# Performance work log

Hardware: AMD Instinct MI355X
Metric: run time of the kernel (lower is better)

Reference implementation:

```python
import jax, jax.numpy as jnp
import numpy as np

N_NODES = 1024
H = 256        # hidden_dim
HEADS = 4
EPS = 1e-5     # torch LayerNorm default


def _ln(x, g, b):
    m = x.mean(-1, keepdims=True)
    v = ((x - m) ** 2).mean(-1, keepdims=True)
    return (x - m) / jnp.sqrt(v + EPS) * g + b


def setup_inputs() -> dict:
    key = jax.random.key(0)
    ks = jax.random.split(key, 24)
    B, L = 16, 64
    P = N_NODES * (N_NODES - 1) // 2
    D0 = L + 7  # latent_dim + 7 stats
    s = 0.02
    f32 = jnp.float32
    d = {}
    d['x'] = jax.random.normal(ks[0], (B, L), f32)
    d['stats'] = jax.random.normal(ks[1], (B, 7), f32)
    d['u'] = jax.random.uniform(ks[2], (B, P, 2), f32)  # uniform noise -> gumbel
    d['ln0_g'] = jnp.ones((D0,), f32); d['ln0_b'] = jnp.zeros((D0,), f32)
    # residual block 1 (in D0 -> H, has projection)
    d['rb1_ln_g'] = jnp.ones((D0,), f32); d['rb1_ln_b'] = jnp.zeros((D0,), f32)
    d['rb1_w1'] = jax.random.normal(ks[3], (H, D0), f32) * s; d['rb1_b1'] = jnp.zeros((H,), f32)
    d['rb1_w2'] = jax.random.normal(ks[4], (H, H), f32) * s;  d['rb1_b2'] = jnp.zeros((H,), f32)
    d['rb1_wp'] = jax.random.normal(ks[5], (H, D0), f32) * s; d['rb1_bp'] = jnp.zeros((H,), f32)
    # residual block 2 (H -> H, no projection)
    d['rb2_ln_g'] = jnp.ones((H,), f32); d['rb2_ln_b'] = jnp.zeros((H,), f32)
    d['rb2_w1'] = jax.random.normal(ks[6], (H, H), f32) * s; d['rb2_b1'] = jnp.zeros((H,), f32)
    d['rb2_w2'] = jax.random.normal(ks[7], (H, H), f32) * s; d['rb2_b2'] = jnp.zeros((H,), f32)
    # GraphAttention: LN + MHA(in_proj, out_proj) + output Linear
    d['att_ln_g'] = jnp.ones((H,), f32); d['att_ln_b'] = jnp.zeros((H,), f32)
    d['att_win'] = jax.random.normal(ks[8], (3 * H, H), f32) * s; d['att_bin'] = jnp.zeros((3 * H,), f32)
    d['att_wout'] = jax.random.normal(ks[9], (H, H), f32) * s;    d['att_bout'] = jnp.zeros((H,), f32)
    d['out_w'] = jax.random.normal(ks[10], (H, H), f32) * s;      d['out_b'] = jnp.zeros((H,), f32)
    # final edge-logit layer over concat([h_i, h_j]) -> 2
    d['fin_w'] = jax.random.normal(ks[11], (2, 2 * H), f32) * s;  d['fin_b'] = jnp.zeros((2,), f32)
    d['temp'] = jnp.ones((1,), f32)
    return d


def reference(x, stats, u, ln0_g, ln0_b,
              rb1_ln_g, rb1_ln_b, rb1_w1, rb1_b1, rb1_w2, rb1_b2, rb1_wp, rb1_bp,
              rb2_ln_g, rb2_ln_b, rb2_w1, rb2_b1, rb2_w2, rb2_b2,
              att_ln_g, att_ln_b, att_win, att_bin, att_wout, att_bout,
              out_w, out_b, fin_w, fin_b, temp):
    B = x.shape[0]
    z = jnp.concatenate([x, stats], axis=-1)          # [B, D0]
    z = _ln(z, ln0_g, ln0_b)
    h = jnp.broadcast_to(z[:, None, :], (B, N_NODES, z.shape[-1]))  # [B, N, D0]
    # residual block 1 (dropout in eval mode = identity)
    t = _ln(h, rb1_ln_g, rb1_ln_b)
    t = jax.nn.gelu(t @ rb1_w1.T + rb1_b1, approximate=False)
    t = t @ rb1_w2.T + rb1_b2
    h = t + (h @ rb1_wp.T + rb1_bp)                   # [B, N, H]
    # residual block 2
    t = _ln(h, rb2_ln_g, rb2_ln_b)
    t = jax.nn.gelu(t @ rb2_w1.T + rb2_b1, approximate=False)
    t = t @ rb2_w2.T + rb2_b2
    h = t + h
    # GraphAttention: LN -> self MHA -> output linear
    a = _ln(h, att_ln_g, att_ln_b)
    qkv = a @ att_win.T + att_bin                      # [B, N, 3H]
    q, k, v = jnp.split(qkv, 3, axis=-1)
    dh = H // HEADS
    def heads(t):
        return t.reshape(B, N_NODES, HEADS, dh).transpose(0, 2, 1, 3)
    q, k, v = heads(q), heads(k), heads(v)
    scores = jnp.einsum('bhqd,bhkd->bhqk', q, k) * np.float32(1.0 / np.sqrt(dh))
    att = jax.nn.softmax(scores, axis=-1)
    o = jnp.einsum('bhqk,bhkd->bhqd', att, v).transpose(0, 2, 1, 3).reshape(B, N_NODES, H)
    o = o @ att_wout.T + att_bout
    h = o @ out_w.T + out_b                            # [B, N, H]
    # pairwise edge logits: Linear(cat(h_i, h_j)) == h_i @ W_a^T + h_j @ W_b^T + b
    la = h @ fin_w[:, :H].T                            # [B, N, 2]
    lb = h @ fin_w[:, H:].T                            # [B, N, 2]
    iu, ju = jnp.triu_indices(N_NODES, k=1)
    logits = la[:, iu] + lb[:, ju] + fin_b             # [B, P, 2]
    # gumbel-softmax (hard, straight-through), tau = |temperature|
    tau = jnp.abs(temp)[0]
    g = -jnp.log(-jnp.log(u + 1e-10) + 1e-10)
    y_soft = jax.nn.softmax((logits + g) / tau, axis=-1)
    y_hard = jax.nn.one_hot(jnp.argmax(y_soft, axis=-1), 2, dtype=y_soft.dtype)
    y = y_hard + y_soft - jax.lax.stop_gradient(y_soft)
    e = y[..., 0]                                      # [B, P]
    adj = jnp.zeros((B, N_NODES, N_NODES), e.dtype).at[:, iu, ju].set(e)
    return adj + adj.transpose(0, 2, 1)
```

## Files before the change

### kernel.cpp

```cpp
#include <hip/hip_runtime.h>
#include <math.h>


#define NN    1024
#define HD    256
#define DIN0  71
#define NPAIR 523776
#define TILE  64
#define NT    16

__device__ __forceinline__ double bred(double v, double* red4) {
  #pragma unroll
  for (int m = 32; m > 0; m >>= 1) v += __shfl_xor(v, m, 64);
  const int wid = threadIdx.x >> 6;
  __syncthreads();
  if ((threadIdx.x & 63) == 0) red4[wid] = v;
  __syncthreads();
  return (red4[0] + red4[1]) + (red4[2] + red4[3]);
}

__device__ __forceinline__ double quad_sum(double v) {
  v += __shfl_xor(v, 1, 64);
  v += __shfl_xor(v, 2, 64);
  return v;
}

__device__ __forceinline__ double dotq256(const double* s,
                                          const float* __restrict__ W,
                                          int row, int p) {
  const float4* w4 = reinterpret_cast<const float4*>(W + (size_t)row * 256);
  double a0 = 0.0, a1 = 0.0, a2 = 0.0, a3 = 0.0;
  #pragma unroll
  for (int k = 0; k < 16; ++k) {
    const int f = p + 4 * k;
    float4 w = w4[f];
    const double* sp = s + 4 * f;
    a0 += sp[0] * (double)w.x;
    a1 += sp[1] * (double)w.y;
    a2 += sp[2] * (double)w.z;
    a3 += sp[3] * (double)w.w;
  }
  return (a0 + a1) + (a2 + a3);
}

__device__ __forceinline__ double dotq71(const double* s,
                                         const float* __restrict__ W,
                                         int row, int p) {
  const float* wr = W + (size_t)row * DIN0;
  double a = 0.0;
  #pragma unroll
  for (int i = p; i < DIN0; i += 4) a += s[i] * (double)wr[i];
  return a;
}

__device__ __forceinline__ double gelu_exact(double x) {
  return 0.5 * x * (1.0 + erf(x * 0.70710678118654752440));
}

__device__ __forceinline__ void ln0_into(const float* __restrict__ x,
                                         const float* __restrict__ stats,
                                         const float* __restrict__ g,
                                         const float* __restrict__ bb,
                                         int b, double* h0, double* red4) {
  const int tid = threadIdx.x;
  double z = 0.0;
  if (tid < DIN0)
    z = (tid < 64) ? (double)x[b * 64 + tid] : (double)stats[b * 7 + tid - 64];
  const double m = bred((tid < DIN0) ? z : 0.0, red4) / (double)DIN0;
  const double d = (tid < DIN0) ? (z - m) : 0.0;
  const double var = bred(d * d, red4) / (double)DIN0;
  const double inv = 1.0 / sqrt(var + (double)1e-5f);
  if (tid < DIN0) h0[tid] = d * inv * (double)g[tid] + (double)bb[tid];
  __syncthreads();
}

__global__ __launch_bounds__(256)
void k1_ln_w1(const float* __restrict__ x, const float* __restrict__ stats,
              const float* __restrict__ ln0_g, const float* __restrict__ ln0_b,
              const float* __restrict__ l1g, const float* __restrict__ l1b,
              const float* __restrict__ W1, const float* __restrict__ b1,
              double* __restrict__ G) {
  __shared__ double t[DIN0], red[4];
  const int b = blockIdx.x >> 2, rg = blockIdx.x & 3;
  const int tid = threadIdx.x;
  ln0_into(x, stats, ln0_g, ln0_b, b, t, red);
  {
    double v = (tid < DIN0) ? t[tid] : 0.0;
    const double m = bred(v, red) / (double)DIN0;
    const double d = (tid < DIN0) ? (t[tid] - m) : 0.0;
    const double var = bred(d * d, red) / (double)DIN0;
    const double inv = 1.0 / sqrt(var + (double)1e-5f);
    __syncthreads();
    if (tid < DIN0) t[tid] = d * inv * (double)l1g[tid] + (double)l1b[tid];
    __syncthreads();
  }
  const int row = rg * 64 + (tid >> 2), p = tid & 3;
  const double d = quad_sum(dotq71(t, W1, row, p));
  if (p == 0) G[b * HD + row] = gelu_exact(d + (double)b1[row]);
}

__global__ __launch_bounds__(256)
void k2_w2_wp(const float* __restrict__ x, const float* __restrict__ stats,
              const float* __restrict__ ln0_g, const float* __restrict__ ln0_b,
              const float* __restrict__ W2, const float* __restrict__ b2,
              const float* __restrict__ Wp, const float* __restrict__ bp,
              const double* __restrict__ G, double* __restrict__ H) {
  __shared__ double h0[DIN0], gs[HD], red[4];
  const int b = blockIdx.x >> 2, rg = blockIdx.x & 3;
  const int tid = threadIdx.x;
  gs[tid] = G[b * HD + tid];
  ln0_into(x, stats, ln0_g, ln0_b, b, h0, red);
  const int row = rg * 64 + (tid >> 2), p = tid & 3;
  const double d2 = quad_sum(dotq256(gs, W2, row, p));
  const double dp = quad_sum(dotq71(h0, Wp, row, p));
  if (p == 0)
    H[b * HD + row] = (d2 + (double)b2[row]) + (dp + (double)bp[row]);
}

__global__ __launch_bounds__(256)
void k3_ln_mv(const double* __restrict__ S,
              const float* __restrict__ lg, const float* __restrict__ lb,
              const float* __restrict__ W, const float* __restrict__ bb,
              double* __restrict__ D, int gelu_flag) {
  __shared__ double t[HD], red[4];
  const int b = blockIdx.x >> 2, rg = blockIdx.x & 3;
  const int tid = threadIdx.x;
  const double s = S[b * HD + tid];
  const double m = bred(s, red) / (double)HD;
  const double d = s - m;
  const double var = bred(d * d, red) / (double)HD;
  const double inv = 1.0 / sqrt(var + (double)1e-5f);
  t[tid] = d * inv * (double)lg[tid] + (double)lb[tid];
  __syncthreads();
  const int row = rg * 64 + (tid >> 2), p = tid & 3;
  const double dd = quad_sum(dotq256(t, W, row, p));
  if (p == 0) {
    const double v = dd + (double)bb[row];
    D[b * HD + row] = gelu_flag ? gelu_exact(v) : v;
  }
}

__global__ __launch_bounds__(256)
void k4_mv_res(const double* __restrict__ G, const float* __restrict__ W,
               const float* __restrict__ bb, double* __restrict__ H) {
  __shared__ double gs[HD];
  const int b = blockIdx.x >> 2, rg = blockIdx.x & 3;
  const int tid = threadIdx.x;
  gs[tid] = G[b * HD + tid];
  __syncthreads();
  const int row = rg * 64 + (tid >> 2), p = tid & 3;
  const double d = quad_sum(dotq256(gs, W, row, p));
  if (p == 0) H[b * HD + row] += d + (double)bb[row];
}

__global__ __launch_bounds__(256)
void k5_mv(const double* __restrict__ S, const float* __restrict__ W,
           const float* __restrict__ bb, double* __restrict__ D) {
  __shared__ double ss[HD];
  const int b = blockIdx.x >> 2, rg = blockIdx.x & 3;
  const int tid = threadIdx.x;
  ss[tid] = S[b * HD + tid];
  __syncthreads();
  const int row = rg * 64 + (tid >> 2), p = tid & 3;
  const double d = quad_sum(dotq256(ss, W, row, p));
  if (p == 0) D[b * HD + row] = d + (double)bb[row];
}

__global__ __launch_bounds__(256)
void k6_fin(const double* __restrict__ Hf, const float* __restrict__ fin_w,
            const float* __restrict__ fin_b, double* __restrict__ c_out) {
  __shared__ double red[4];
  const int b = blockIdx.x;
  const int tid = threadIdx.x;
  const double hj = Hf[b * HD + tid];
  const double v0 = hj * (double)fin_w[tid]          + hj * (double)fin_w[HD + tid];
  const double v1 = hj * (double)fin_w[2 * HD + tid] + hj * (double)fin_w[3 * HD + tid];
  const double c0 = bred(v0, red) + (double)fin_b[0];
  const double c1 = bred(v1, red) + (double)fin_b[1];
  if (tid == 0) {
    c_out[2 * b + 0] = c0;
    c_out[2 * b + 1] = c1;
  }
}

__global__ __launch_bounds__(256)
void adj_tile_kernel(const float* __restrict__ u, const double* __restrict__ c,
                     float* __restrict__ out) {
  __shared__ float tile[TILE][TILE + 1];
  const int b = blockIdx.y;
  int k = blockIdx.x;
  int ti = 0;
  while (k >= NT - ti) { k -= NT - ti; ++ti; }
  const int tj = ti + k;
  const bool diag = (ti == tj);

  const int t        = threadIdx.x;
  const int lane_col = (t & 15) << 2;
  const int row_base = t >> 4;
  const double c0 = c[2 * b + 0];
  const double c1 = c[2 * b + 1];
  const float* ub = u + (size_t)b * (2u * NPAIR);
  float* ob = out + ((size_t)b << 20);

  #pragma unroll
  for (int s = 0; s < 4; ++s) {
    const int il = s * 16 + row_base;
    const int i  = ti * TILE + il;
    const int rb = i * (2 * NN - 1 - i) / 2 - i - 1;
    float4 ev4;
    float* ev = &ev4.x;
    #pragma unroll
    for (int q = 0; q < 4; ++q) {
      const int jl = lane_col + q;
      const int j  = tj * TILE + jl;
      float e = 0.0f;
      if (j > i) {
        const int p2 = rb + j;
        const float2 uu = *reinterpret_cast<const float2*>(ub + 2 * p2);
        const float g0 = -logf(-logf(uu.x + 1e-10f) + 1e-10f);
        const float g1 = -logf(-logf(uu.y + 1e-10f) + 1e-10f);
        e = ((c0 + (double)g0) >= (c1 + (double)g1)) ? 1.0f : 0.0f;
      }
      ev[q] = e;
      tile[il][jl] = e;
    }
    if (!diag) {
      *reinterpret_cast<float4*>(ob + (size_t)i * NN + tj * TILE + lane_col) = ev4;
    }
  }
  __syncthreads();

  #pragma unroll
  for (int s = 0; s < 4; ++s) {
    const int rl = s * 16 + row_base;
    if (!diag) {
      float4 v = make_float4(tile[lane_col + 0][rl], tile[lane_col + 1][rl],
                             tile[lane_col + 2][rl], tile[lane_col + 3][rl]);
      *reinterpret_cast<float4*>(ob + (size_t)(tj * TILE + rl) * NN
                                    + ti * TILE + lane_col) = v;
    } else {
      float v[4];
      #pragma unroll
      for (int q = 0; q < 4; ++q) {
        const int jl = lane_col + q;
        v[q] = (jl > rl) ? tile[rl][jl] : ((jl < rl) ? tile[jl][rl] : 0.0f);
      }
      *reinterpret_cast<float4*>(ob + (size_t)(ti * TILE + rl) * NN
                                    + ti * TILE + lane_col)
          = make_float4(v[0], v[1], v[2], v[3]);
    }
  }
}

extern "C" void kernel_launch(void* const* d_in, const int* in_sizes, int n_in,
                              void* d_out, int out_size, void* d_ws, size_t ws_size,
                              hipStream_t stream) {
  const float* x        = (const float*)d_in[0];
  const float* stats    = (const float*)d_in[1];
  const float* u        = (const float*)d_in[2];
  const float* ln0_g    = (const float*)d_in[3];
  const float* ln0_b    = (const float*)d_in[4];
  const float* rb1_ln_g = (const float*)d_in[5];
  const float* rb1_ln_b = (const float*)d_in[6];
  const float* rb1_w1   = (const float*)d_in[7];
  const float* rb1_b1   = (const float*)d_in[8];
  const float* rb1_w2   = (const float*)d_in[9];
  const float* rb1_b2   = (const float*)d_in[10];
  const float* rb1_wp   = (const float*)d_in[11];
  const float* rb1_bp   = (const float*)d_in[12];
  const float* rb2_ln_g = (const float*)d_in[13];
  const float* rb2_ln_b = (const float*)d_in[14];
  const float* rb2_w1   = (const float*)d_in[15];
  const float* rb2_b1   = (const float*)d_in[16];
  const float* rb2_w2   = (const float*)d_in[17];
  const float* rb2_b2   = (const float*)d_in[18];
  const float* att_ln_g = (const float*)d_in[19];
  const float* att_ln_b = (const float*)d_in[20];
  const float* att_win  = (const float*)d_in[21];
  const float* att_bin  = (const float*)d_in[22];
  const float* att_wout = (const float*)d_in[23];
  const float* att_bout = (const float*)d_in[24];
  const float* out_w    = (const float*)d_in[25];
  const float* out_b    = (const float*)d_in[26];
  const float* fin_w    = (const float*)d_in[27];
  const float* fin_b    = (const float*)d_in[28];

  float* out   = (float*)d_out;
  double* c_ws = (double*)d_ws;

  double* G = (double*)(out + ((size_t)16 * NN * NN - 3 * 16 * HD * 2));
  double* H = G + 16 * HD;
  double* T = H + 16 * HD;

  const dim3 g64(64), t256(256);
  hipLaunchKernelGGL(k1_ln_w1, g64, t256, 0, stream,
                     x, stats, ln0_g, ln0_b, rb1_ln_g, rb1_ln_b,
                     rb1_w1, rb1_b1, G);
  hipLaunchKernelGGL(k2_w2_wp, g64, t256, 0, stream,
                     x, stats, ln0_g, ln0_b, rb1_w2, rb1_b2, rb1_wp, rb1_bp,
                     G, H);
  hipLaunchKernelGGL(k3_ln_mv, g64, t256, 0, stream,
                     H, rb2_ln_g, rb2_ln_b, rb2_w1, rb2_b1, G, 1);
  hipLaunchKernelGGL(k4_mv_res, g64, t256, 0, stream,
                     G, rb2_w2, rb2_b2, H);
  hipLaunchKernelGGL(k3_ln_mv, g64, t256, 0, stream,
                     H, att_ln_g, att_ln_b, att_win + 2 * HD * HD,
                     att_bin + 2 * HD, G, 0);
  hipLaunchKernelGGL(k5_mv, g64, t256, 0, stream, G, att_wout, att_bout, T);
  hipLaunchKernelGGL(k5_mv, g64, t256, 0, stream, T, out_w, out_b, G);
  hipLaunchKernelGGL(k6_fin, dim3(16), t256, 0, stream, G, fin_w, fin_b, c_ws);

  hipLaunchKernelGGL(adj_tile_kernel, dim3(NT * (NT + 1) / 2, 16), t256, 0, stream,
                     u, c_ws, out);
}
```

Before: 223.6 us.

## Fuse head MLP chain into cooperative kernel and batch nontemporal loads in adjacency tiles

Replaces the eight small head kernels with one cooperative kernel that uses grid-wide syncs between stages, and falls back to the old launches if the cooperative launch fails. This removes per-launch overhead and the gaps between the small dependent kernels. The adjacency kernel now splits the off-diagonal and diagonal paths. On the off-diagonal path it issues all 16 noise loads up front and uses nontemporal loads and stores to cut cache pollution on the big output. In exchange, grid syncs carry their own cost, and the head stage only runs 64 blocks.

```diff
diff --git a/kernel.cpp b/kernel.cpp
--- a/kernel.cpp
+++ b/kernel.cpp
@@ -1,5 +1,8 @@
 #include <hip/hip_runtime.h>
+#include <hip/hip_cooperative_groups.h>
 #include <math.h>
+
+namespace cg = cooperative_groups;
 
 
 #define NN    1024
@@ -8,6 +11,9 @@
 #define NPAIR 523776
 #define TILE  64
 #define NT    16
+
+typedef float f32x2 __attribute__((ext_vector_type(2)));
+typedef float f32x4 __attribute__((ext_vector_type(4)));
 
 __device__ __forceinline__ double bred(double v, double* red4) {
   #pragma unroll
@@ -74,6 +80,123 @@
   __syncthreads();
 }
 
+__device__ __forceinline__ void ln256_into(const double* __restrict__ S, int b,
+                                           const float* __restrict__ lg,
+                                           const float* __restrict__ lb,
+                                           double* dst, double* red4) {
+  const int tid = threadIdx.x;
+  const double s = S[b * HD + tid];
+  const double m = bred(s, red4) / (double)HD;
+  const double d = s - m;
+  const double var = bred(d * d, red4) / (double)HD;
+  const double inv = 1.0 / sqrt(var + (double)1e-5f);
+  dst[tid] = d * inv * (double)lg[tid] + (double)lb[tid];
+  __syncthreads();
+}
+
+__global__ __launch_bounds__(256)
+void head_coop(const float* __restrict__ x, const float* __restrict__ stats,
+               const float* __restrict__ ln0_g, const float* __restrict__ ln0_b,
+               const float* __restrict__ rb1_ln_g, const float* __restrict__ rb1_ln_b,
+               const float* __restrict__ rb1_w1, const float* __restrict__ rb1_b1,
+               const float* __restrict__ rb1_w2, const float* __restrict__ rb1_b2,
+               const float* __restrict__ rb1_wp, const float* __restrict__ rb1_bp,
+               const float* __restrict__ rb2_ln_g, const float* __restrict__ rb2_ln_b,
+               const float* __restrict__ rb2_w1, const float* __restrict__ rb2_b1,
+               const float* __restrict__ rb2_w2, const float* __restrict__ rb2_b2,
+               const float* __restrict__ att_ln_g, const float* __restrict__ att_ln_b,
+               const float* __restrict__ att_win_v, const float* __restrict__ att_bin_v,
+               const float* __restrict__ att_wout, const float* __restrict__ att_bout,
+               const float* __restrict__ out_w, const float* __restrict__ out_b,
+               const float* __restrict__ fin_w, const float* __restrict__ fin_b,
+               double* __restrict__ G, double* __restrict__ H,
+               double* __restrict__ T, double* __restrict__ c_out) {
+  cg::grid_group grid = cg::this_grid();
+  __shared__ double sv[HD], h0[DIN0], red[4];
+  const int tid = threadIdx.x;
+  const int b = blockIdx.x >> 2, rg = blockIdx.x & 3;
+  const int row = rg * 64 + (tid >> 2), p = tid & 3;
+
+#define GSYNC() do { __threadfence(); grid.sync(); __threadfence(); } while (0)
+
+  ln0_into(x, stats, ln0_g, ln0_b, b, h0, red);
+  {
+    double v = (tid < DIN0) ? h0[tid] : 0.0;
+    const double m = bred(v, red) / (double)DIN0;
+    const double d = (tid < DIN0) ? (h0[tid] - m) : 0.0;
+    const double var = bred(d * d, red) / (double)DIN0;
+    const double inv = 1.0 / sqrt(var + (double)1e-5f);
+    if (tid < DIN0) sv[tid] = d * inv * (double)rb1_ln_g[tid] + (double)rb1_ln_b[tid];
+    __syncthreads();
+  }
+  {
+    const double d = quad_sum(dotq71(sv, rb1_w1, row, p));
+    if (p == 0) G[b * HD + row] = gelu_exact(d + (double)rb1_b1[row]);
+  }
+  GSYNC();
+
+  sv[tid] = G[b * HD + tid];
+  __syncthreads();
+  {
+    const double d2 = quad_sum(dotq256(sv, rb1_w2, row, p));
+    const double dp = quad_sum(dotq71(h0, rb1_wp, row, p));
+    if (p == 0)
+      H[b * HD + row] = (d2 + (double)rb1_b2[row]) + (dp + (double)rb1_bp[row]);
+  }
+  GSYNC();
+
+  ln256_into(H, b, rb2_ln_g, rb2_ln_b, sv, red);
+  {
+    const double d = quad_sum(dotq256(sv, rb2_w1, row, p));
+    if (p == 0) G[b * HD + row] = gelu_exact(d + (double)rb2_b1[row]);
+  }
+  GSYNC();
+
+  sv[tid] = G[b * HD + tid];
+  __syncthreads();
+  {
+    const double d = quad_sum(dotq256(sv, rb2_w2, row, p));
+    if (p == 0) H[b * HD + row] += d + (double)rb2_b2[row];
+  }
+  GSYNC();
+
+  ln256_into(H, b, att_ln_g, att_ln_b, sv, red);
+  {
+    const double d = quad_sum(dotq256(sv, att_win_v, row, p));
+    if (p == 0) G[b * HD + row] = d + (double)att_bin_v[row];
+  }
+  GSYNC();
+
+  sv[tid] = G[b * HD + tid];
+  __syncthreads();
+  {
+    const double d = quad_sum(dotq256(sv, att_wout, row, p));
+    if (p == 0) T[b * HD + row] = d + (double)att_bout[row];
+  }
+  GSYNC();
+
+  sv[tid] = T[b * HD + tid];
+  __syncthreads();
+  {
+    const double d = quad_sum(dotq256(sv, out_w, row, p));
+    if (p == 0) G[b * HD + row] = d + (double)out_b[row];
+  }
+  GSYNC();
+
+  if (rg == 0) {
+    const double hj = G[b * HD + tid];
+    const double v0 = hj * (double)fin_w[tid]          + hj * (double)fin_w[HD + tid];
+    const double v1 = hj * (double)fin_w[2 * HD + tid] + hj * (double)fin_w[3 * HD + tid];
+    const double c0 = bred(v0, red) + (double)fin_b[0];
+    const double c1 = bred(v1, red) + (double)fin_b[1];
+    if (tid == 0) {
+      c_out[2 * b + 0] = c0;
+      c_out[2 * b + 1] = c1;
+    }
+  }
+#undef GSYNC
+}
+
 __global__ __launch_bounds__(256)
 void k1_ln_w1(const float* __restrict__ x, const float* __restrict__ stats,
               const float* __restrict__ ln0_g, const float* __restrict__ ln0_b,
@@ -124,15 +247,8 @@
               double* __restrict__ D, int gelu_flag) {
   __shared__ double t[HD], red[4];
   const int b = blockIdx.x >> 2, rg = blockIdx.x & 3;
-  const int tid = threadIdx.x;
-  const double s = S[b * HD + tid];
-  const double m = bred(s, red) / (double)HD;
-  const double d = s - m;
-  const double var = bred(d * d, red) / (double)HD;
-  const double inv = 1.0 / sqrt(var + (double)1e-5f);
-  t[tid] = d * inv * (double)lg[tid] + (double)lb[tid];
-  __syncthreads();
-  const int row = rg * 64 + (tid >> 2), p = tid & 3;
+  ln256_into(S, b, lg, lb, t, red);
+  const int row = rg * 64 + (threadIdx.x >> 2), p = threadIdx.x & 3;
   const double dd = quad_sum(dotq256(t, W, row, p));
   if (p == 0) {
     const double v = dd + (double)bb[row];
@@ -192,7 +308,6 @@
   int ti = 0;
   while (k >= NT - ti) { k -= NT - ti; ++ti; }
   const int tj = ti + k;
-  const bool diag = (ti == tj);
 
   const int t        = threadIdx.x;
   const int lane_col = (t & 15) << 2;
@@ -202,52 +317,84 @@
   const float* ub = u + (size_t)b * (2u * NPAIR);
   float* ob = out + ((size_t)b << 20);
 
-  #pragma unroll
-  for (int s = 0; s < 4; ++s) {
-    const int il = s * 16 + row_base;
-    const int i  = ti * TILE + il;
-    const int rb = i * (2 * NN - 1 - i) / 2 - i - 1;
-    float4 ev4;
-    float* ev = &ev4.x;
-    #pragma unroll
-    for (int q = 0; q < 4; ++q) {
-      const int jl = lane_col + q;
-      const int j  = tj * TILE + jl;
-      float e = 0.0f;
-      if (j > i) {
-        const int p2 = rb + j;
-        const float2 uu = *reinterpret_cast<const float2*>(ub + 2 * p2);
+  if (ti != tj) {
+    int pb[4];
+    #pragma unroll
+    for (int s = 0; s < 4; ++s) {
+      const int i = ti * TILE + s * 16 + row_base;
+      pb[s] = i * (2 * NN - 1 - i) / 2 - i - 1 + tj * TILE + lane_col;
+    }
+    f32x2 r[16];
+    #pragma unroll
+    for (int s = 0; s < 4; ++s)
+      #pragma unroll
+      for (int q = 0; q < 4; ++q)
+        r[s * 4 + q] = __builtin_nontemporal_load(
+            reinterpret_cast<const f32x2*>(ub + 2 * (pb[s] + q)));
+    #pragma unroll
+    for (int s = 0; s < 4; ++s) {
+      const int il = s * 16 + row_base;
+      f32x4 ev4;
+      #pragma unroll
+      for (int q = 0; q < 4; ++q) {
+        const f32x2 uu = r[s * 4 + q];
         const float g0 = -logf(-logf(uu.x + 1e-10f) + 1e-10f);
         const float g1 = -logf(-logf(uu.y + 1e-10f) + 1e-10f);
-        e = ((c0 + (double)g0) >= (c1 + (double)g1)) ? 1.0f : 0.0f;
+        const float e = ((c0 + (double)g0) >= (c1 + (double)g1)) ? 1.0f : 0.0f;
+        ev4[q] = e;
+        tile[il][lane_col + q] = e;
       }
-      ev[q] = e;
-      tile[il][jl] = e;
-    }
-    if (!diag) {
-      *reinterpret_cast<float4*>(ob + (size_t)i * NN + tj * TILE + lane_col) = ev4;
-    }
-  }
-  __syncthreads();
-
-  #pragma unroll
-  for (int s = 0; s < 4; ++s) {
-    const int rl = s * 16 + row_base;
-    if (!diag) {
-      float4 v = make_float4(tile[lane_col + 0][rl], tile[lane_col + 1][rl],
-                             tile[lane_col + 2][rl], tile[lane_col + 3][rl]);
-      *reinterpret_cast<float4*>(ob + (size_t)(tj * TILE + rl) * NN
-                                    + ti * TILE + lane_col) = v;
-    } else {
-      float v[4];
+      const int i = ti * TILE + il;
+      __builtin_nontemporal_store(ev4,
+          reinterpret_cast<f32x4*>(ob + (size_t)i * NN + tj * TILE + lane_col));
+    }
+    __syncthreads();
+    #pragma unroll
+    for (int s = 0; s < 4; ++s) {
+      const int rl = s * 16 + row_base;
+      f32x4 v;
+      v[0] = tile[lane_col + 0][rl];
+      v[1] = tile[lane_col + 1][rl];
+      v[2] = tile[lane_col + 2][rl];
+      v[3] = tile[lane_col + 3][rl];
+      __builtin_nontemporal_store(v,
+          reinterpret_cast<f32x4*>(ob + (size_t)(tj * TILE + rl) * NN
+                                      + ti * TILE + lane_col));
+    }
+  } else {
+    #pragma unroll
+    for (int s = 0; s < 4; ++s) {
+      const int il = s * 16 + row_base;
+      const int i  = ti * TILE + il;
+      const int rb = i * (2 * NN - 1 - i) / 2 - i - 1;
+      #pragma unroll
+      for (int q = 0; q < 4; ++q) {
+        const int jl = lane_col + q;
+        const int j  = tj * TILE + jl;
+        float e = 0.0f;
+        if (j > i) {
+          const int p2 = rb + j;
+          const float2 uu = *reinterpret_cast<const float2*>(ub + 2 * p2);
+          const float g0 = -logf(-logf(uu.x + 1e-10f) + 1e-10f);
+          const float g1 = -logf(-logf(uu.y + 1e-10f) + 1e-10f);
+          e = ((c0 + (double)g0) >= (c1 + (double)g1)) ? 1.0f : 0.0f;
+        }
+        tile[il][jl] = e;
+      }
+    }
+    __syncthreads();
+    #pragma unroll
+    for (int s = 0; s < 4; ++s) {
+      const int rl = s * 16 + row_base;
+      f32x4 v;
       #pragma unroll
       for (int q = 0; q < 4; ++q) {
         const int jl = lane_col + q;
         v[q] = (jl > rl) ? tile[rl][jl] : ((jl < rl) ? tile[jl][rl] : 0.0f);
       }
-      *reinterpret_cast<float4*>(ob + (size_t)(ti * TILE + rl) * NN
-                                    + ti * TILE + lane_col)
-          = make_float4(v[0], v[1], v[2], v[3]);
+      __builtin_nontemporal_store(v,
+          reinterpret_cast<f32x4*>(ob + (size_t)(ti * TILE + rl) * NN
+                                      + ti * TILE + lane_col));
     }
   }
 }
@@ -292,24 +439,41 @@
   double* H = G + 16 * HD;
   double* T = H + 16 * HD;
 
-  const dim3 g64(64), t256(256);
-  hipLaunchKernelGGL(k1_ln_w1, g64, t256, 0, stream,
-                     x, stats, ln0_g, ln0_b, rb1_ln_g, rb1_ln_b,
-                     rb1_w1, rb1_b1, G);
-  hipLaunchKernelGGL(k2_w2_wp, g64, t256, 0, stream,
-                     x, stats, ln0_g, ln0_b, rb1_w2, rb1_b2, rb1_wp, rb1_bp,
-                     G, H);
-  hipLaunchKernelGGL(k3_ln_mv, g64, t256, 0, stream,
-                     H, rb2_ln_g, rb2_ln_b, rb2_w1, rb2_b1, G, 1);
-  hipLaunchKernelGGL(k4_mv_res, g64, t256, 0, stream,
-                     G, rb2_w2, rb2_b2, H);
-  hipLaunchKernelGGL(k3_ln_mv, g64, t256, 0, stream,
-                     H, att_ln_g, att_ln_b, att_win + 2 * HD * HD,
-                     att_bin + 2 * HD, G, 0);
-  hipLaunchKernelGGL(k5_mv, g64, t256, 0, stream, G, att_wout, att_bout, T);
-  hipLaunchKernelGGL(k5_mv, g64, t256, 0, stream, T, out_w, out_b, G);
-  hipLaunchKernelGGL(k6_fin, dim3(16), t256, 0, stream, G, fin_w, fin_b, c_ws);
-
-  hipLaunchKernelGGL(adj_tile_kernel, dim3(NT * (NT + 1) / 2, 16), t256, 0, stream,
-                     u, c_ws, out);
-}
+  const float* att_win_v = att_win + 2 * HD * HD;
+  const float* att_bin_v = att_bin + 2 * HD;
+
+  void* kargs[] = {
+    (void*)&x, (void*)&stats, (void*)&ln0_g, (void*)&ln0_b,
+    (void*)&rb1_ln_g, (void*)&rb1_ln_b, (void*)&rb1_w1, (void*)&rb1_b1,
+    (void*)&rb1_w2, (void*)&rb1_b2, (void*)&rb1_wp, (void*)&rb1_bp,
+    (void*)&rb2_ln_g, (void*)&rb2_ln_b, (void*)&rb2_w1, (void*)&rb2_b1,
+    (void*)&rb2_w2, (void*)&rb2_b2, (void*)&att_ln_g, (void*)&att_ln_b,
+    (void*)&att_win_v, (void*)&att_bin_v, (void*)&att_wout, (void*)&att_bout,
+    (void*)&out_w, (void*)&out_b, (void*)&fin_w, (void*)&fin_b,
+    (void*)&G, (void*)&H, (void*)&T, (void*)&c_ws
+  };
+  hipError_t cerr = hipLaunchCooperativeKernel(
+      reinterpret_cast<void*>(head_coop), dim3(64), dim3(256), kargs, 0, stream);
+
+  if (cerr != hipSuccess) {
+    const dim3 g64(64), t256(256);
+    hipLaunchKernelGGL(k1_ln_w1, g64, t256, 0, stream,
+                       x, stats, ln0_g, ln0_b, rb1_ln_g, rb1_ln_b,
+                       rb1_w1, rb1_b1, G);
+    hipLaunchKernelGGL(k2_w2_wp, g64, t256, 0, stream,
+                       x, stats, ln0_g, ln0_b, rb1_w2, rb1_b2, rb1_wp, rb1_bp,
+                       G, H);
+    hipLaunchKernelGGL(k3_ln_mv, g64, t256, 0, stream,
+                       H, rb2_ln_g, rb2_ln_b, rb2_w1, rb2_b1, G, 1);
+    hipLaunchKernelGGL(k4_mv_res, g64, t256, 0, stream,
+                       G, rb2_w2, rb2_b2, H);
+    hipLaunchKernelGGL(k3_ln_mv, g64, t256, 0, stream,
+                       H, att_ln_g, att_ln_b, att_win_v, att_bin_v, G, 0);
+    hipLaunchKernelGGL(k5_mv, g64, t256, 0, stream, G, att_wout, att_bout, T);
+    hipLaunchKernelGGL(k5_mv, g64, t256, 0, stream, T, out_w, out_b, G);
+    hipLaunchKernelGGL(k6_fin, dim3(16), t256, 0, stream, G, fin_w, fin_b, c_ws);
+  }
+
+  hipLaunchKernelGGL(adj_tile_kernel, dim3(NT * (NT + 1) / 2, 16), dim3(256),
+                     0, stream, u, c_ws, out);
+}
```

Measured after the change: 384.7 us. 72.1% more time.
